# Performance work log

Hardware: AMD Instinct MI355X
Metric: run time of the kernel (lower is better)

## Reference

```python
import jax, jax.numpy as jnp
import numpy as np


def setup_inputs() -> dict:
    key = jax.random.key(0)
    k1, k2, k3, k4, k5 = jax.random.split(key, 5)
    B, C, H, W = 4, 256, 64, 64
    INTER = 128
    # NOTE: original inits out.weight to zeros (residual identity at init);
    # we use small random weights so the reference exercises the full math.
    s = 0.02
    return {
        "x": jax.random.normal(k1, (B, C, H, W), dtype=jnp.float32),
        "w_theta": jax.random.normal(k2, (INTER, C), dtype=jnp.float32) * s,
        "w_phi": jax.random.normal(k3, (INTER, C), dtype=jnp.float32) * s,
        "w_g": jax.random.normal(k4, (INTER, C), dtype=jnp.float32) * s,
        "w_out": jax.random.normal(k5, (C, INTER), dtype=jnp.float32) * s,
    }


def reference(x, w_theta, w_phi, w_g, w_out):
    B, C, H, W = x.shape
    N = H * W
    xf = x.reshape(B, C, N)                      # [B, C, N]
    theta = jnp.einsum("ic,bcn->bni", w_theta, xf)  # [B, N, inter]
    phi = jnp.einsum("ic,bcn->bin", w_phi, xf)      # [B, inter, N]
    g = jnp.einsum("ic,bcn->bni", w_g, xf)          # [B, N, inter]
    attn = jax.nn.softmax(jnp.einsum("bni,bim->bnm", theta, phi), axis=-1)  # [B, N, N]
    y = jnp.einsum("bnm,bmi->bin", attn, g)         # [B, inter, N]
    out = jnp.einsum("ci,bin->bcn", w_out, y)       # [B, C, N]
    return x + out.reshape(B, C, H, W)
```

## Files before the change

kernel.cpp:

```cpp
#include <hip/hip_runtime.h>
#include <hip/hip_bf16.h>
#include <cstdint>

#define BATCH 4
#define CDIM 256
#define NTOK 4096
#define IDIM 128

typedef __attribute__((ext_vector_type(4))) float f32x4;
typedef __attribute__((ext_vector_type(16))) float f32x16;
typedef __attribute__((ext_vector_type(8))) short short8;

static __device__ __forceinline__ unsigned cvt_pk(float lo, float hi) {
  unsigned r;
  asm("v_cvt_pk_bf16_f32 %0, %1, %2" : "=v"(r) : "v"(lo), "v"(hi));
  return r;
}
static __device__ __forceinline__ float bf2f(unsigned short u) {
  union { unsigned u; float f; } v;
  v.u = (unsigned)u << 16;
  return v.f;
}
static __device__ __forceinline__ float exp2_f(float x) {
#if __has_builtin(__builtin_amdgcn_exp2f)
  return __builtin_amdgcn_exp2f(x);
#else
  return exp2f(x);
#endif
}
static __device__ __forceinline__ void gl16(const void* g, void* l) {
  __builtin_amdgcn_global_load_lds(
      (const __attribute__((address_space(1))) void*)g,
      (__attribute__((address_space(3))) void*)l, 16, 0, 0);
}

__global__ __launch_bounds__(256) void cast_w_kernel(
    const float* __restrict__ wt, const float* __restrict__ wp,
    const float* __restrict__ wg, const float* __restrict__ wo,
    unsigned short* __restrict__ Wb)
{
  int id = blockIdx.x * 256 + threadIdx.x;
  if (id < 24576) {
    int pidx = id >> 13;
    int rem = id & 8191;
    int i = rem >> 6, c4 = (rem & 63) * 4;
    const float* src = pidx == 0 ? wt : pidx == 1 ? wp : wg;
    float4 v = *(const float4*)&src[i * 256 + c4];
    float s = (pidx == 0) ? 1.4426950408889634f : 1.0f;
    uint2 u = make_uint2(cvt_pk(v.x * s, v.y * s), cvt_pk(v.z * s, v.w * s));
    *(uint2*)&Wb[(((size_t)pidx * 32 + (c4 >> 3)) * 128 + i) * 8 + (c4 & 7)] = u;
  } else {
    int rem = id - 24576;
    int c = rem >> 5, i4 = (rem & 31) * 4;
    float4 v = *(const float4*)&wo[c * 128 + i4];
    uint2 u = make_uint2(cvt_pk(v.x, v.y), cvt_pk(v.z, v.w));
    *(uint2*)&Wb[98304 + (((size_t)(i4 >> 3) * 256 + c) * 8) + (i4 & 7)] = u;
  }
}

__global__ __launch_bounds__(768) void qkv_kernel(
    const float* __restrict__ x, const unsigned short* __restrict__ Wb,
    unsigned short* __restrict__ Q, unsigned short* __restrict__ K,
    unsigned short* __restrict__ Vt)
{
  __shared__ __align__(16) unsigned short xt[64 * 256];
  __shared__ __align__(16) unsigned short sc[8][16 * 128];

  const int b = blockIdx.y;
  const int n0 = blockIdx.x * 64;
  const int t = threadIdx.x;
  const float* xb = x + (size_t)b * CDIM * NTOK;

  for (int it = 0; it < 3; ++it) {
    int u = it * 768 + t;
    if (u < 2048) {
      int c0 = (u >> 4) * 2;
      int n4 = (u & 15) * 4;
      float4 va = *(const float4*)&xb[(size_t)c0 * NTOK + n0 + n4];
      float4 vb = *(const float4*)&xb[(size_t)(c0 + 1) * NTOK + n0 + n4];
      const float* pa = (const float*)&va;
      const float* pb = (const float*)&vb;
#pragma unroll
      for (int j = 0; j < 4; ++j) {
        int n = n4 + j;
        unsigned pk = cvt_pk(pa[j], pb[j]);
        *(unsigned*)((char*)xt + n * 512 + ((c0 * 2) ^ ((n & 15) << 4))) = pk;
      }
    }
  }
  __syncthreads();

  const int lane = t & 63;
  const int wv = __builtin_amdgcn_readfirstlane(t >> 6);
  const int nsub = wv & 3, proj = wv >> 2;
  const int cl = lane & 15, g = lane >> 4;

  f32x4 acc[8];
#pragma unroll
  for (int i = 0; i < 8; ++i) acc[i] = (f32x4){0.f, 0.f, 0.f, 0.f};

  const int nrow = nsub * 16 + cl;
  const int swz = (nrow & 15) << 4;
#pragma unroll
  for (int kc = 0; kc < 8; ++kc) {
    int cb = kc * 32 + g * 8;
    short8 af = *(const short8*)((const char*)xt + nrow * 512 + ((cb * 2) ^ swz));
#pragma unroll
    for (int is = 0; is < 8; ++is) {
      short8 bf = *(const short8*)&Wb[(((size_t)proj * 32 + kc * 4 + g) * 128 +
                                       is * 16 + cl) * 8];
      acc[is] = __builtin_amdgcn_mfma_f32_16x16x32_bf16(af, bf, acc[is], 0, 0, 0);
    }
  }

  if (proj < 2) {
    unsigned short* scw = sc[wv];
#pragma unroll
    for (int is = 0; is < 8; ++is)
#pragma unroll
      for (int r = 0; r < 4; ++r) {
        int nl = g * 4 + r;
        int i2 = (is * 16 + cl) * 2;
        *(unsigned short*)((char*)scw + nl * 256 + (i2 ^ ((nl & 15) << 4))) =
            (unsigned short)cvt_pk(acc[is][r], 0.f);
      }
    unsigned short* dst = (proj == 0 ? Q : K) +
        ((size_t)b * NTOK + n0 + nsub * 16) * IDIM;
    int nr = lane >> 2;
    int swr = (nr & 15) << 4;
#pragma unroll
    for (int j = 0; j < 4; ++j) {
      int ch = (lane & 3) + 4 * j;
      short8 v = *(const short8*)((const char*)scw + nr * 256 + ((ch * 16) ^ swr));
      *(short8*)&dst[(size_t)nr * IDIM + ch * 8] = v;
    }
  } else {
    unsigned short* dstV = Vt + (size_t)b * IDIM * NTOK + n0 + nsub * 16 + g * 4;
#pragma unroll
    for (int is = 0; is < 8; ++is) {
      uint2 u = make_uint2(cvt_pk(acc[is][0], acc[is][1]),
                           cvt_pk(acc[is][2], acc[is][3]));
      *(uint2*)&dstV[(size_t)(is * 16 + cl) * NTOK] = u;
    }
  }
}

__global__ __launch_bounds__(128, 2) void attn_kernel(
    const unsigned short* __restrict__ Q, const unsigned short* __restrict__ K,
    const unsigned short* __restrict__ Vt, unsigned short* __restrict__ Op,
    float2* __restrict__ ML)
{
  __shared__ __align__(16) unsigned short kls[2][32 * 128];
  __shared__ __align__(16) unsigned short vls[2][128 * 32];

  const int bid = blockIdx.x;
  const int b = (bid >> 1) & 3;
  const int ms = (bid >> 3) & 3;
  const int nblk = (bid >> 5) + (bid & 1) * 32;
  const int t = threadIdx.x;
  const int lane = t & 63;
  const int wv = __builtin_amdgcn_readfirstlane(t >> 6);
  const int n0 = nblk * 64 + wv * 32;
  const int c32 = lane & 31, hl = lane >> 5;
  const int p = t;

  const unsigned short* Kb = K + (size_t)b * NTOK * IDIM;
  const unsigned short* Vb = Vt + (size_t)b * IDIM * NTOK;

  const unsigned short* Qp = Q + ((size_t)b * NTOK + n0 + c32) * IDIM + hl * 8;
  short8 q[8];
#pragma unroll
  for (int kc = 0; kc < 8; ++kc) q[kc] = *(const short8*)(Qp + kc * 16);

  f32x16 o[4];
#pragma unroll
  for (int it = 0; it < 4; ++it)
#pragma unroll
    for (int e = 0; e < 16; ++e) o[it][e] = 0.f;
  float M = -3.0e38f, L = 0.f;

  const int idxswap = ((lane ^ 32) & 63) * 4;

#define STAGE(cb, m0_)                                                        \
  {                                                                           \
    _Pragma("unroll")                                                         \
    for (int u = 0; u < 4; ++u) {                                             \
      int idx = p + 128 * u;                                                  \
      int r = idx >> 4, ch = idx & 15;                                        \
      gl16(Kb + (size_t)((m0_) + r) * IDIM + ((ch ^ (r & 7)) * 8),            \
           (void*)&kls[cb][idx * 8]);                                         \
    }                                                                         \
    _Pragma("unroll")                                                         \
    for (int u = 0; u < 4; ++u) {                                             \
      int idx = p + 128 * u;                                                  \
      int i = idx >> 2, mc = idx & 3;                                         \
      gl16(Vb + (size_t)i * NTOK + (m0_) + ((mc ^ (i & 3)) * 8),              \
           (void*)&vls[cb][idx * 8]);                                         \
    }                                                                         \
  }

  const int mbase = ms * 1024;
  STAGE(0, mbase)

  for (int tt = 0; tt < 32; ++tt) {
    asm volatile("s_waitcnt vmcnt(0) lgkmcnt(0)\n\ts_barrier" ::: "memory");
    if (tt < 31) STAGE((tt + 1) & 1, mbase + (tt + 1) * 32)

    const char* kbuf = (const char*)kls[tt & 1];
    const char* vbuf = (const char*)vls[tt & 1];

    f32x16 st;
#pragma unroll
    for (int e = 0; e < 16; ++e) st[e] = 0.f;
    __builtin_amdgcn_s_setprio(1);
#pragma unroll
    for (int kc = 0; kc < 8; ++kc) {
      short8 kf = *(const short8*)(kbuf + c32 * 256 +
                                   ((kc * 32 + hl * 16) ^ ((c32 & 7) << 4)));
      st = __builtin_amdgcn_mfma_f32_32x32x16_bf16(kf, q[kc], st, 0, 0, 0);
    }
    __builtin_amdgcn_s_setprio(0);

    float sm = st[0];
#pragma unroll
    for (int e = 1; e < 16; ++e) sm = fmaxf(sm, st[e]);
    sm = fmaxf(sm, __shfl_xor(sm, 32));
    if (!__all(sm <= M + 11.5f)) {
      float Mn = fmaxf(M, sm);
      float scl = exp2_f(M - Mn);
      M = Mn;
      L *= scl;
#pragma unroll
      for (int it = 0; it < 4; ++it)
#pragma unroll
        for (int e = 0; e < 16; ++e) o[it][e] *= scl;
    }
    float pr[16];
#pragma unroll
    for (int e = 0; e < 16; ++e) pr[e] = exp2_f(st[e] - M);
    float ls = 0.f;
#pragma unroll
    for (int e = 0; e < 16; ++e) ls += pr[e];
    ls += __shfl_xor(ls, 32);
    L += ls;

    short8 pf[2];
#pragma unroll
    for (int kt = 0; kt < 2; ++kt) {
      unsigned a0 = cvt_pk(pr[kt * 8 + 0], pr[kt * 8 + 1]);
      unsigned a1 = cvt_pk(pr[kt * 8 + 2], pr[kt * 8 + 3]);
      unsigned a2 = cvt_pk(pr[kt * 8 + 4], pr[kt * 8 + 5]);
      unsigned a3 = cvt_pk(pr[kt * 8 + 6], pr[kt * 8 + 7]);
      unsigned x0 = (unsigned)__builtin_amdgcn_ds_bpermute(idxswap, (int)a0);
      unsigned x1 = (unsigned)__builtin_amdgcn_ds_bpermute(idxswap, (int)a1);
      unsigned x2 = (unsigned)__builtin_amdgcn_ds_bpermute(idxswap, (int)a2);
      unsigned x3 = (unsigned)__builtin_amdgcn_ds_bpermute(idxswap, (int)a3);
      union { unsigned u[4]; short8 s; } w;
      w.u[0] = hl ? x2 : a0;
      w.u[1] = hl ? x3 : a1;
      w.u[2] = hl ? a2 : x0;
      w.u[3] = hl ? a3 : x1;
      pf[kt] = w.s;
    }

    __builtin_amdgcn_s_setprio(1);
#pragma unroll
    for (int it = 0; it < 4; ++it) {
#pragma unroll
      for (int kt = 0; kt < 2; ++kt) {
        int row = it * 32 + c32;
        short8 vf = *(const short8*)(vbuf + row * 64 +
                                     ((kt * 32 + hl * 16) ^ ((row & 3) << 4)));
        o[it] = __builtin_amdgcn_mfma_f32_32x32x16_bf16(vf, pf[kt], o[it], 0, 0, 0);
      }
    }
    __builtin_amdgcn_s_setprio(0);
  }
#undef STAGE

  {
    const int sb = ms * 4 + b;
    unsigned short* Ob = Op + (size_t)sb * (16 * NTOK * 8);
#pragma unroll
    for (int it = 0; it < 4; ++it)
#pragma unroll
      for (int g2 = 0; g2 < 4; ++g2) {
        uint2 u2 = make_uint2(cvt_pk(o[it][4 * g2 + 0], o[it][4 * g2 + 1]),
                              cvt_pk(o[it][4 * g2 + 2], o[it][4 * g2 + 3]));
        *(uint2*)&Ob[((size_t)(it * 4 + g2) * NTOK + n0 + c32) * 8 + 4 * hl] = u2;
      }
    if (hl == 0) ML[(size_t)sb * NTOK + n0 + c32] = make_float2(M, L);
  }
}

__global__ __launch_bounds__(256) void out_kernel(
    const float* __restrict__ x, const unsigned short* __restrict__ Wb,
    const unsigned short* __restrict__ Op, const float2* __restrict__ ML,
    float* __restrict__ out)
{
  const int b = blockIdx.y;
  const int n0 = blockIdx.x * 32;
  const int t = threadIdx.x;
  const int lane = t & 63;
  const int wv = __builtin_amdgcn_readfirstlane(t >> 6);
  const int cl = lane & 15, g = lane >> 4;

  float ws4[2][4];
#pragma unroll
  for (int nsb = 0; nsb < 2; ++nsb) {
    int n = n0 + nsb * 16 + cl;
    float2 m0 = ML[(size_t)(0 * 4 + b) * NTOK + n];
    float2 m1 = ML[(size_t)(1 * 4 + b) * NTOK + n];
    float2 m2 = ML[(size_t)(2 * 4 + b) * NTOK + n];
    float2 m3 = ML[(size_t)(3 * 4 + b) * NTOK + n];
    float Mx = fmaxf(fmaxf(m0.x, m1.x), fmaxf(m2.x, m3.x));
    float w0 = exp2_f(m0.x - Mx), w1 = exp2_f(m1.x - Mx);
    float w2 = exp2_f(m2.x - Mx), w3 = exp2_f(m3.x - Mx);
    float rinv = 1.f / (w0 * m0.y + w1 * m1.y + w2 * m2.y + w3 * m3.y);
    ws4[nsb][0] = w0 * rinv; ws4[nsb][1] = w1 * rinv;
    ws4[nsb][2] = w2 * rinv; ws4[nsb][3] = w3 * rinv;
  }

  f32x4 acc[4][2];
#pragma unroll
  for (int cs = 0; cs < 4; ++cs)
#pragma unroll
    for (int nsb = 0; nsb < 2; ++nsb) acc[cs][nsb] = (f32x4){0.f, 0.f, 0.f, 0.f};

#pragma unroll
  for (int kc = 0; kc < 4; ++kc) {
    short8 bf[2];
#pragma unroll
    for (int nsb = 0; nsb < 2; ++nsb) {
      int n = n0 + nsb * 16 + cl;
      size_t base = ((size_t)(kc * 4 + g) * NTOK + n) * 8;
      const short8 f0 = *(const short8*)&Op[(size_t)(0 * 4 + b) * (16 * NTOK * 8) + base];
      const short8 f1 = *(const short8*)&Op[(size_t)(1 * 4 + b) * (16 * NTOK * 8) + base];
      const short8 f2 = *(const short8*)&Op[(size_t)(2 * 4 + b) * (16 * NTOK * 8) + base];
      const short8 f3 = *(const short8*)&Op[(size_t)(3 * 4 + b) * (16 * NTOK * 8) + base];
      float a[8];
#pragma unroll
      for (int e = 0; e < 8; ++e)
        a[e] = ws4[nsb][0] * bf2f((unsigned short)f0[e]) +
               ws4[nsb][1] * bf2f((unsigned short)f1[e]) +
               ws4[nsb][2] * bf2f((unsigned short)f2[e]) +
               ws4[nsb][3] * bf2f((unsigned short)f3[e]);
      union { unsigned u[4]; short8 s; } r;
#pragma unroll
      for (int jp = 0; jp < 4; ++jp) r.u[jp] = cvt_pk(a[2 * jp], a[2 * jp + 1]);
      bf[nsb] = r.s;
    }
#pragma unroll
    for (int cs = 0; cs < 4; ++cs) {
      short8 af = *(const short8*)&Wb[98304 +
          (((size_t)(kc * 4 + g)) * 256 + wv * 64 + cs * 16 + cl) * 8];
#pragma unroll
      for (int nsb = 0; nsb < 2; ++nsb)
        acc[cs][nsb] = __builtin_amdgcn_mfma_f32_16x16x32_bf16(af, bf[nsb], acc[cs][nsb], 0, 0, 0);
    }
  }

  const float* xb = x + (size_t)b * CDIM * NTOK;
  float* ob = out + (size_t)b * CDIM * NTOK;
#pragma unroll
  for (int cs = 0; cs < 4; ++cs)
#pragma unroll
    for (int nsb = 0; nsb < 2; ++nsb)
#pragma unroll
      for (int r = 0; r < 4; ++r) {
        int c = wv * 64 + cs * 16 + g * 4 + r;
        int n = n0 + nsb * 16 + cl;
        ob[(size_t)c * NTOK + n] = xb[(size_t)c * NTOK + n] + acc[cs][nsb][r];
      }
}

extern "C" void kernel_launch(void* const* d_in, const int* in_sizes, int n_in,
                              void* d_out, int out_size, void* d_ws, size_t ws_size,
                              hipStream_t stream) {
  const float* x  = (const float*)d_in[0];
  const float* wt = (const float*)d_in[1];
  const float* wp = (const float*)d_in[2];
  const float* wg = (const float*)d_in[3];
  const float* wo = (const float*)d_in[4];
  float* outp = (float*)d_out;

  char* ws = (char*)d_ws;
  unsigned short* Wb  = (unsigned short*)(ws);
  unsigned short* Qd  = (unsigned short*)(ws + (size_t)1  * (1 << 20));
  unsigned short* Kd  = (unsigned short*)(ws + (size_t)5  * (1 << 20));
  unsigned short* Vtd = (unsigned short*)(ws + (size_t)9  * (1 << 20));
  unsigned short* Opd = (unsigned short*)(ws + (size_t)13 * (1 << 20));
  float2* MLd         = (float2*)(ws + (size_t)29 * (1 << 20));

  cast_w_kernel<<<128, 256, 0, stream>>>(wt, wp, wg, wo, Wb);
  qkv_kernel<<<dim3(64, BATCH), 768, 0, stream>>>(x, Wb, Qd, Kd, Vtd);
  attn_kernel<<<1024, 128, 0, stream>>>(Qd, Kd, Vtd, Opd, MLd);
  out_kernel<<<dim3(128, BATCH), 256, 0, stream>>>(x, Wb, Opd, MLd, outp);
}
```

Baseline: 87.03 us.

## Precompute LDS/global offsets, re-swizzle V tile, split QK accumulators, use permlane32 swap

Hoists all LDS and global address arithmetic for the K/V staging and fragment loads into per-thread offset arrays computed once. Changes the V tile LDS layout to a 128-byte-row swizzle that pairs rows to cut bank conflicts. Splits the QK^T MFMA chain into two independent accumulators to shorten the dependency chain, and uses tree reductions for the row max and sum. Replaces the ds_bpermute-based half-wave exchange with v_permlane32_swap, avoiding LDS traffic. Costs extra registers for the offset arrays and the second accumulator.

```diff
diff --git a/kernel.cpp b/kernel.cpp
--- a/kernel.cpp
+++ b/kernel.cpp
@@ -172,6 +172,31 @@
 #pragma unroll
   for (int kc = 0; kc < 8; ++kc) q[kc] = *(const short8*)(Qp + kc * 16);
 
+  int koff[8];
+#pragma unroll
+  for (int kc = 0; kc < 8; ++kc)
+    koff[kc] = c32 * 256 + ((((kc * 2 + hl) ^ (c32 & 7))) << 4);
+  int voff[8];
+#pragma unroll
+  for (int it = 0; it < 4; ++it)
+#pragma unroll
+    for (int kt = 0; kt < 2; ++kt) {
+      int rp = it * 16 + (c32 >> 1);
+      voff[it * 2 + kt] =
+          rp * 128 + ((((c32 & 1) * 4 + kt * 2 + hl) ^ (rp & 7)) << 4);
+    }
+  int kgo[4], vgo[4], lofs[4];
+#pragma unroll
+  for (int u = 0; u < 4; ++u) {
+    int idx = p + 128 * u;
+    lofs[u] = idx * 16;
+    int r = idx >> 4, ch = idx & 15;
+    kgo[u] = r * IDIM + ((ch ^ (r & 7)) * 8);
+    int rp = idx >> 3, pp = idx & 7;
+    int s = pp ^ (rp & 7);
+    vgo[u] = (rp * 2 + (s >> 2)) * NTOK + (s & 3) * 8;
+  }
+
   f32x16 o[4];
 #pragma unroll
   for (int it = 0; it < 4; ++it)
@@ -179,24 +204,16 @@
     for (int e = 0; e < 16; ++e) o[it][e] = 0.f;
   float M = -3.0e38f, L = 0.f;
 
-  const int idxswap = ((lane ^ 32) & 63) * 4;
-
 #define STAGE(cb, m0_)                                                        \
   {                                                                           \
+    const unsigned short* Kit = Kb + (size_t)(m0_)*IDIM;                      \
+    const unsigned short* Vit = Vb + (m0_);                                   \
     _Pragma("unroll")                                                         \
-    for (int u = 0; u < 4; ++u) {                                             \
-      int idx = p + 128 * u;                                                  \
-      int r = idx >> 4, ch = idx & 15;                                        \
-      gl16(Kb + (size_t)((m0_) + r) * IDIM + ((ch ^ (r & 7)) * 8),            \
-           (void*)&kls[cb][idx * 8]);                                         \
-    }                                                                         \
+    for (int u = 0; u < 4; ++u)                                               \
+      gl16(Kit + kgo[u], (char*)kls[cb] + lofs[u]);                           \
     _Pragma("unroll")                                                         \
-    for (int u = 0; u < 4; ++u) {                                             \
-      int idx = p + 128 * u;                                                  \
-      int i = idx >> 2, mc = idx & 3;                                         \
-      gl16(Vb + (size_t)i * NTOK + (m0_) + ((mc ^ (i & 3)) * 8),              \
-           (void*)&vls[cb][idx * 8]);                                         \
-    }                                                                         \
+    for (int u = 0; u < 4; ++u)                                               \
+      gl16(Vit + vgo[u], (char*)vls[cb] + lofs[u]);                           \
   }
 
   const int mbase = ms * 1024;
@@ -209,21 +226,26 @@
     const char* kbuf = (const char*)kls[tt & 1];
     const char* vbuf = (const char*)vls[tt & 1];
 
-    f32x16 st;
-#pragma unroll
-    for (int e = 0; e < 16; ++e) st[e] = 0.f;
+    f32x16 sa, sb;
+#pragma unroll
+    for (int e = 0; e < 16; ++e) { sa[e] = 0.f; sb[e] = 0.f; }
     __builtin_amdgcn_s_setprio(1);
 #pragma unroll
-    for (int kc = 0; kc < 8; ++kc) {
-      short8 kf = *(const short8*)(kbuf + c32 * 256 +
-                                   ((kc * 32 + hl * 16) ^ ((c32 & 7) << 4)));
-      st = __builtin_amdgcn_mfma_f32_32x32x16_bf16(kf, q[kc], st, 0, 0, 0);
+    for (int kc = 0; kc < 4; ++kc) {
+      short8 ka = *(const short8*)(kbuf + koff[kc]);
+      short8 kb2 = *(const short8*)(kbuf + koff[kc + 4]);
+      sa = __builtin_amdgcn_mfma_f32_32x32x16_bf16(ka, q[kc], sa, 0, 0, 0);
+      sb = __builtin_amdgcn_mfma_f32_32x32x16_bf16(kb2, q[kc + 4], sb, 0, 0, 0);
     }
     __builtin_amdgcn_s_setprio(0);
-
-    float sm = st[0];
-#pragma unroll
-    for (int e = 1; e < 16; ++e) sm = fmaxf(sm, st[e]);
+    f32x16 st = sa + sb;
+
+    float mx[8];
+#pragma unroll
+    for (int j = 0; j < 8; ++j) mx[j] = fmaxf(st[j], st[j + 8]);
+#pragma unroll
+    for (int j = 0; j < 4; ++j) mx[j] = fmaxf(mx[j], mx[j + 4]);
+    float sm = fmaxf(fmaxf(mx[0], mx[1]), fmaxf(mx[2], mx[3]));
     sm = fmaxf(sm, __shfl_xor(sm, 32));
     if (!__all(sm <= M + 11.5f)) {
       float Mn = fmaxf(M, sm);
@@ -238,9 +260,12 @@
     float pr[16];
 #pragma unroll
     for (int e = 0; e < 16; ++e) pr[e] = exp2_f(st[e] - M);
-    float ls = 0.f;
-#pragma unroll
-    for (int e = 0; e < 16; ++e) ls += pr[e];
+    float sv[8];
+#pragma unroll
+    for (int j = 0; j < 8; ++j) sv[j] = pr[j] + pr[j + 8];
+#pragma unroll
+    for (int j = 0; j < 4; ++j) sv[j] += sv[j + 4];
+    float ls = (sv[0] + sv[1]) + (sv[2] + sv[3]);
     ls += __shfl_xor(ls, 32);
     L += ls;
 
@@ -251,15 +276,10 @@
       unsigned a1 = cvt_pk(pr[kt * 8 + 2], pr[kt * 8 + 3]);
       unsigned a2 = cvt_pk(pr[kt * 8 + 4], pr[kt * 8 + 5]);
       unsigned a3 = cvt_pk(pr[kt * 8 + 6], pr[kt * 8 + 7]);
-      unsigned x0 = (unsigned)__builtin_amdgcn_ds_bpermute(idxswap, (int)a0);
-      unsigned x1 = (unsigned)__builtin_amdgcn_ds_bpermute(idxswap, (int)a1);
-      unsigned x2 = (unsigned)__builtin_amdgcn_ds_bpermute(idxswap, (int)a2);
-      unsigned x3 = (unsigned)__builtin_amdgcn_ds_bpermute(idxswap, (int)a3);
+      asm volatile("v_permlane32_swap_b32 %0, %1" : "+v"(a0), "+v"(a2));
+      asm volatile("v_permlane32_swap_b32 %0, %1" : "+v"(a1), "+v"(a3));
       union { unsigned u[4]; short8 s; } w;
-      w.u[0] = hl ? x2 : a0;
-      w.u[1] = hl ? x3 : a1;
-      w.u[2] = hl ? a2 : x0;
-      w.u[3] = hl ? a3 : x1;
+      w.u[0] = a0; w.u[1] = a1; w.u[2] = a2; w.u[3] = a3;
       pf[kt] = w.s;
     }
 
@@ -268,9 +288,7 @@
     for (int it = 0; it < 4; ++it) {
 #pragma unroll
       for (int kt = 0; kt < 2; ++kt) {
-        int row = it * 32 + c32;
-        short8 vf = *(const short8*)(vbuf + row * 64 +
-                                     ((kt * 32 + hl * 16) ^ ((row & 3) << 4)));
+        short8 vf = *(const short8*)(vbuf + voff[it * 2 + kt]);
         o[it] = __builtin_amdgcn_mfma_f32_32x32x16_bf16(vf, pf[kt], o[it], 0, 0, 0);
       }
     }
@@ -279,8 +297,8 @@
 #undef STAGE
 
   {
-    const int sb = ms * 4 + b;
-    unsigned short* Ob = Op + (size_t)sb * (16 * NTOK * 8);
+    const int sb2 = ms * 4 + b;
+    unsigned short* Ob = Op + (size_t)sb2 * (16 * NTOK * 8);
 #pragma unroll
     for (int it = 0; it < 4; ++it)
 #pragma unroll
@@ -289,7 +307,7 @@
                               cvt_pk(o[it][4 * g2 + 2], o[it][4 * g2 + 3]));
         *(uint2*)&Ob[((size_t)(it * 4 + g2) * NTOK + n0 + c32) * 8 + 4 * hl] = u2;
       }
-    if (hl == 0) ML[(size_t)sb * NTOK + n0 + c32] = make_float2(M, L);
+    if (hl == 0) ML[(size_t)sb2 * NTOK + n0 + c32] = make_float2(M, L);
   }
 }
 
```

Result: faster. 80.92 us (-7.0%).
